# Optimization experiments

Measured on AMD Instinct MI355X. Metric: run time of the kernel, lower is better.

The kernel has to match this reference:

```python
import jax, jax.numpy as jnp
import numpy as np

B, L, D = 32, 256, 1024
ALIGN = 1024
FF = 2048
NUM_CLASSES = 3


def setup_inputs() -> dict:
    key = jax.random.key(0)
    ks = jax.random.split(key, 10)
    u = lambda k, shape: jax.random.uniform(k, shape, jnp.float32, -1.0, 1.0)
    return {
        "premises": jax.random.normal(ks[0], (B, L, D), jnp.float32),
        "hypotheses": jax.random.normal(ks[1], (B, L, D), jnp.float32),
        "W_F": u(ks[2], (D, ALIGN)),
        "W_G": u(ks[3], (2 * D, FF)),
        "W1": u(ks[4], (2 * FF, FF)) * 0.02,
        "b1": jnp.zeros((FF,), jnp.float32),
        "W2": u(ks[5], (FF, FF)) * 0.02,
        "b2": jnp.zeros((FF,), jnp.float32),
        "W3": u(ks[6], (FF, NUM_CLASSES)) * 0.02,
        "b3": jnp.zeros((NUM_CLASSES,), jnp.float32),
    }


def reference(premises, hypotheses, W_F, W_G, W1, b1, W2, b2, W3, b3):
    # ---- align: tanh-projected cross attention ----
    F_p = jnp.tanh(jnp.einsum("bpd,da->bpa", premises, W_F))      # [B,Lp,A]
    F_h = jnp.tanh(jnp.einsum("bhd,da->bha", hypotheses, W_F))    # [B,Lh,A]
    eijs = jnp.einsum("bpa,bha->bph", F_p, F_h)                   # [B,Lp,Lh]
    attn = jax.nn.softmax(eijs, axis=-1)                          # tf.nn.softmax: last axis
    betas = jnp.einsum("bph,bhd->bpd", attn, hypotheses)          # [B,Lp,D]
    alphas = jnp.einsum("bph,bpd->bhd", attn, premises)           # [B,Lh,D]

    # ---- compare (dropout is identity: p_keep = 1.0 at eval) ----
    V1 = jnp.tanh(jnp.concatenate([premises, betas], axis=2) @ W_G)    # [B,Lp,FF]
    V2 = jnp.tanh(jnp.concatenate([hypotheses, alphas], axis=2) @ W_G) # [B,Lh,FF]

    # ---- aggregate: sum-pool over sequence, concat ----
    agg = jnp.concatenate([V1.sum(axis=1), V2.sum(axis=1)], axis=1)    # [B,2*FF]

    # ---- classifier MLP ----
    a1 = jnp.tanh(agg @ W1 + b1)
    a2 = jnp.tanh(a1 @ W2 + b2)
    logits = a2 @ W3 + b3                                              # [B,3]
    return logits
```

## Files before the change

### kernel.cpp

```cpp
#include <hip/hip_runtime.h>
#include <hip/hip_bf16.h>
#include <stdint.h>


typedef __attribute__((ext_vector_type(8))) short    short8_t;
typedef __attribute__((ext_vector_type(4))) float    float4_t;
typedef __attribute__((ext_vector_type(8))) _Float16 half8_t;
typedef __attribute__((ext_vector_type(4))) _Float16 half4_t;

#define DEVI static __device__ __forceinline__

DEVI short f2bf(float f) {
  union { float f; unsigned u; } v; v.f = f;
  unsigned r = v.u + 0x7fffu + ((v.u >> 16) & 1u);
  return (short)(r >> 16);
}
DEVI float bf2f(short s) {
  union { unsigned u; float f; } v;
  v.u = ((unsigned)(unsigned short)s) << 16;
  return v.f;
}
DEVI void split2(float x, short& hi, short& lo) {
  hi = f2bf(x);
  lo = f2bf(x - bf2f(hi));
}
DEVI float fast_tanh(float x) {
  float e = __expf(2.0f * x);
  return 1.0f - 2.0f / (e + 1.0f);
}
DEVI void gload16(const void* g, void* l) {
  __builtin_amdgcn_global_load_lds(
      (const __attribute__((address_space(1))) void*)g,
      (__attribute__((address_space(3))) void*)l, 16, 0, 0);
}

template <int DO_TANH, int OUT_MODE>
__global__ __launch_bounds__(256) void gemm_nt_split(
    const short* __restrict__ Ah, const short* __restrict__ Al, int lda, long sA,
    const short* __restrict__ Bh, const short* __restrict__ Bl, int ldb, long sB,
    void* __restrict__ Ch, void* __restrict__ Cl, int ldc, long sC,
    int M, int K, int kslices)
{
  __shared__ __align__(16) short Ash[128][40];
  __shared__ __align__(16) short Asl[128][40];
  __shared__ __align__(16) short Bsh[128][40];
  __shared__ __align__(16) short Bsl[128][40];

  const int z  = blockIdx.z;
  const int zb = z / kslices;
  const int zk = z - zb * kslices;
  const int Ksub = K / kslices;
  const int kbeg = zk * Ksub, kend = kbeg + Ksub;

  Ah += (size_t)zb * sA;  Al += (size_t)zb * sA;
  Bh += (size_t)zb * sB;  Bl += (size_t)zb * sB;

  const int row0 = blockIdx.x * 128;
  const int col0 = blockIdx.y * 128;

  const int t    = threadIdx.x;
  const int lane = t & 63;
  const int wave = t >> 6;
  const int wr = wave >> 1, wc = wave & 1;
  const int m15 = lane & 15, q = lane >> 4;

  float4_t acc[4][4];
#pragma unroll
  for (int i = 0; i < 4; ++i)
#pragma unroll
    for (int j = 0; j < 4; ++j) acc[i][j] = (float4_t)0.0f;

  for (int k0 = kbeg; k0 < kend; k0 += 32) {
#pragma unroll
    for (int i = 0; i < 2; ++i) {
      int c  = t + 256 * i;
      int r  = c >> 2;
      int kc = (c & 3) << 3;
      size_t ao = (size_t)(row0 + r) * lda + k0 + kc;
      size_t bo = (size_t)(col0 + r) * ldb + k0 + kc;
      *(int4*)(&Ash[r][kc]) = *(const int4*)(Ah + ao);
      *(int4*)(&Asl[r][kc]) = *(const int4*)(Al + ao);
      *(int4*)(&Bsh[r][kc]) = *(const int4*)(Bh + bo);
      *(int4*)(&Bsl[r][kc]) = *(const int4*)(Bl + bo);
    }
    __syncthreads();

    short8_t ah[4], al[4];
#pragma unroll
    for (int i = 0; i < 4; ++i) {
      ah[i] = *(const short8_t*)(&Ash[wr * 64 + i * 16 + m15][q * 8]);
      al[i] = *(const short8_t*)(&Asl[wr * 64 + i * 16 + m15][q * 8]);
    }
#pragma unroll
    for (int j = 0; j < 4; ++j) {
      short8_t bh = *(const short8_t*)(&Bsh[wc * 64 + j * 16 + m15][q * 8]);
      short8_t bl = *(const short8_t*)(&Bsl[wc * 64 + j * 16 + m15][q * 8]);
#pragma unroll
      for (int i = 0; i < 4; ++i) {
        acc[i][j] = __builtin_amdgcn_mfma_f32_16x16x32_bf16(ah[i], bh, acc[i][j], 0, 0, 0);
        acc[i][j] = __builtin_amdgcn_mfma_f32_16x16x32_bf16(ah[i], bl, acc[i][j], 0, 0, 0);
        acc[i][j] = __builtin_amdgcn_mfma_f32_16x16x32_bf16(al[i], bh, acc[i][j], 0, 0, 0);
      }
    }
    __syncthreads();
  }

  short* Chs = (short*)Ch + (size_t)zb * sC;
  short* Cls = (short*)Cl + (size_t)zb * sC;
  float* Cf  = (float*)Ch + (size_t)zb * sC;
#pragma unroll
  for (int i = 0; i < 4; ++i) {
#pragma unroll
    for (int r = 0; r < 4; ++r) {
      int gm = row0 + wr * 64 + i * 16 + q * 4 + r;
      if (gm < M) {
#pragma unroll
        for (int j = 0; j < 4; ++j) {
          int gn = col0 + wc * 64 + j * 16 + m15;
          float v = acc[i][j][r];
          if (DO_TANH) v = fast_tanh(v);
          if (OUT_MODE == 0) {
            atomicAdd(&Cf[(size_t)gm * ldc + gn], v);
          } else {
            short hi, lo; split2(v, hi, lo);
            Chs[(size_t)gm * ldc + gn] = hi;
            Cls[(size_t)gm * ldc + gn] = lo;
          }
        }
      }
    }
  }
}

template <int MODE>
__global__ __launch_bounds__(256) void gemm_f16(
    const _Float16* __restrict__ A, int lda, long sA,
    const _Float16* __restrict__ B, int ldb, long sB,
    _Float16* __restrict__ C, int ldc, long sC,
    int K, float* __restrict__ agg)
{
  __shared__ __align__(16) _Float16 As[2 * 128 * 32];
  __shared__ __align__(16) _Float16 Bs[2 * 128 * 32];

  const int z = blockIdx.z;
  A += (size_t)z * sA;
  B += (size_t)z * sB;

  const int row0 = blockIdx.x * 128;
  const int col0 = blockIdx.y * 128;
  const int t = threadIdx.x, lane = t & 63, wave = t >> 6;
  const int wr = wave >> 1, wc = wave & 1;
  const int m15 = lane & 15, q = lane >> 4;

  const int srow = wave * 32 + (lane >> 2);
  const int cg   = ((lane & 3) ^ ((lane >> 3) & 3)) * 8;
  const _Float16* gA0 = A + (size_t)(row0 + srow) * lda + cg;
  const _Float16* gA1 = gA0 + (size_t)16 * lda;
  const _Float16* gB0 = B + (size_t)(col0 + srow) * ldb + cg;
  const _Float16* gB1 = gB0 + (size_t)16 * ldb;
  const _Float16* gA0b = gA0 + 32;
  const _Float16* gA1b = gA1 + 32;
  const _Float16* gB0b = gB0 + 32;
  const _Float16* gB1b = gB1 + 32;
  _Float16* lA0  = &As[(wave * 32) * 32];
  _Float16* lA1  = &As[(wave * 32 + 16) * 32];
  _Float16* lB0  = &Bs[(wave * 32) * 32];
  _Float16* lB1  = &Bs[(wave * 32 + 16) * 32];
  _Float16* lA0b = lA0 + 4096;
  _Float16* lA1b = lA1 + 4096;
  _Float16* lB0b = lB0 + 4096;
  _Float16* lB1b = lB1 + 4096;

  const int fs = (q ^ ((m15 >> 1) & 3)) * 8;
  int aoff[4], boff[4];
#pragma unroll
  for (int i = 0; i < 4; ++i) {
    aoff[i] = (wr * 64 + i * 16 + m15) * 32 + fs;
    boff[i] = (wc * 64 + i * 16 + m15) * 32 + fs;
  }

  float4_t acc[4][4];
#pragma unroll
  for (int i = 0; i < 4; ++i)
#pragma unroll
    for (int j = 0; j < 4; ++j) acc[i][j] = (float4_t)0.0f;

  for (int k0 = 0; k0 < K; k0 += 64) {
    gload16(gA0, lA0);  gload16(gA1, lA1);
    gload16(gB0, lB0);  gload16(gB1, lB1);
    gload16(gA0b, lA0b); gload16(gA1b, lA1b);
    gload16(gB0b, lB0b); gload16(gB1b, lB1b);
    gA0 += 64; gA1 += 64; gB0 += 64; gB1 += 64;
    gA0b += 64; gA1b += 64; gB0b += 64; gB1b += 64;
    __syncthreads();

#pragma unroll
    for (int h = 0; h < 2; ++h) {
      half8_t af[4], bfr[4];
#pragma unroll
      for (int i = 0; i < 4; ++i) af[i]  = *(const half8_t*)&As[h * 4096 + aoff[i]];
#pragma unroll
      for (int j = 0; j < 4; ++j) bfr[j] = *(const half8_t*)&Bs[h * 4096 + boff[j]];
#pragma unroll
      for (int i = 0; i < 4; ++i)
#pragma unroll
        for (int j = 0; j < 4; ++j)
          acc[i][j] = __builtin_amdgcn_mfma_f32_16x16x32_f16(af[i], bfr[j], acc[i][j], 0, 0, 0);
    }
    __syncthreads();
  }

  if (MODE == 2) {
    const int half_ = row0 >= 8192;
    const int b     = (row0 & 8191) >> 8;
#pragma unroll
    for (int j = 0; j < 4; ++j) {
      float s = 0.0f;
#pragma unroll
      for (int i = 0; i < 4; ++i)
#pragma unroll
        for (int r = 0; r < 4; ++r) s += fast_tanh(acc[i][j][r]);
      s += __shfl_xor(s, 16);
      s += __shfl_xor(s, 32);
      if (q == 0) {
        int col = col0 + wc * 64 + j * 16 + m15;
        atomicAdd(&agg[(size_t)b * 4096 + half_ * 2048 + col], s);
      }
    }
  } else {
    _Float16* Cp = C + (size_t)z * sC;
#pragma unroll
    for (int i = 0; i < 4; ++i)
#pragma unroll
      for (int r = 0; r < 4; ++r) {
        int gm = row0 + wr * 64 + i * 16 + q * 4 + r;
#pragma unroll
        for (int j = 0; j < 4; ++j) {
          int gn = col0 + wc * 64 + j * 16 + m15;
          Cp[(size_t)gm * ldc + gn] = (_Float16)acc[i][j][r];
        }
      }
  }
}

__global__ __launch_bounds__(256) void transpose_split(
    const float* __restrict__ in, short* __restrict__ oh, short* __restrict__ ol,
    int R, int C)
{
  __shared__ float tile[32][33];
  const int tx = threadIdx.x & 31, ty = threadIdx.x >> 5;
  const int c0 = blockIdx.x * 32, r0 = blockIdx.y * 32;
#pragma unroll
  for (int i = 0; i < 4; ++i) {
    int r = ty + i * 8;
    tile[r][tx] = in[(size_t)(r0 + r) * C + c0 + tx];
  }
  __syncthreads();
#pragma unroll
  for (int i = 0; i < 4; ++i) {
    int cc = ty + i * 8;
    float v = tile[tx][cc];
    short hi, lo; split2(v, hi, lo);
    size_t o = (size_t)(c0 + cc) * R + r0 + tx;
    oh[o] = hi;
    ol[o] = lo;
  }
}

__global__ __launch_bounds__(256) void transpose_f16(
    const float* __restrict__ in, _Float16* __restrict__ out, int R, int C)
{
  __shared__ float tile[32][33];
  const int tx = threadIdx.x & 31, ty = threadIdx.x >> 5;
  const int c0 = blockIdx.x * 32, r0 = blockIdx.y * 32;
#pragma unroll
  for (int i = 0; i < 4; ++i) {
    int r = ty + i * 8;
    tile[r][tx] = in[(size_t)(r0 + r) * C + c0 + tx];
  }
  __syncthreads();
#pragma unroll
  for (int i = 0; i < 4; ++i) {
    int cc = ty + i * 8;
    out[(size_t)(c0 + cc) * R + r0 + tx] = (_Float16)tile[tx][cc];
  }
}

__global__ __launch_bounds__(256) void transpose_f16_ph(
    const float* __restrict__ P, const float* __restrict__ Hh,
    _Float16* __restrict__ out)
{
  __shared__ float tile[32][33];
  const int zz = blockIdx.z;
  const float* in = (zz < 32 ? P : Hh) + (size_t)(zz & 31) * (256 * 1024);
  _Float16* o = out + (size_t)zz * (1024 * 256);
  const int tx = threadIdx.x & 31, ty = threadIdx.x >> 5;
  const int c0 = blockIdx.x * 32, r0 = blockIdx.y * 32;
#pragma unroll
  for (int i = 0; i < 4; ++i) {
    int r = ty + i * 8;
    tile[r][tx] = in[(size_t)(r0 + r) * 1024 + c0 + tx];
  }
  __syncthreads();
#pragma unroll
  for (int i = 0; i < 4; ++i) {
    int cc = ty + i * 8;
    o[(size_t)(c0 + cc) * 256 + r0 + tx] = (_Float16)tile[tx][cc];
  }
}

__global__ __launch_bounds__(256) void transpose_b2b(
    const short* __restrict__ in, short* __restrict__ out,
    int R, int C, long sIn, long sOut)
{
  __shared__ short tile[32][33];
  in  += (size_t)blockIdx.z * sIn;
  out += (size_t)blockIdx.z * sOut;
  const int tx = threadIdx.x & 31, ty = threadIdx.x >> 5;
  const int c0 = blockIdx.x * 32, r0 = blockIdx.y * 32;
#pragma unroll
  for (int i = 0; i < 4; ++i) {
    int r = ty + i * 8;
    tile[r][tx] = in[(size_t)(r0 + r) * C + c0 + tx];
  }
  __syncthreads();
#pragma unroll
  for (int i = 0; i < 4; ++i) {
    int cc = ty + i * 8;
    out[(size_t)(c0 + cc) * R + r0 + tx] = tile[tx][cc];
  }
}

__global__ __launch_bounds__(256) void conv_in(
    const float* __restrict__ P, const float* __restrict__ Hh,
    short* __restrict__ oh, short* __restrict__ ol, _Float16* __restrict__ cat)
{
  const int zz = blockIdx.z;
  const float* in = zz ? Hh : P;
  oh  += (size_t)zz * 8192 * 1024;
  ol  += (size_t)zz * 8192 * 1024;
  cat += (size_t)zz * 8192 * 2048;
  size_t i = ((size_t)blockIdx.x * 256 + threadIdx.x) * 4;
  float4 v = *(const float4*)&in[i];
  short4 h, l;
  split2(v.x, h.x, l.x); split2(v.y, h.y, l.y);
  split2(v.z, h.z, l.z); split2(v.w, h.w, l.w);
  *(short4*)&oh[i] = h;
  *(short4*)&ol[i] = l;
  size_t row = i >> 10;
  int col    = (int)(i & 1023);
  half4_t c16;
  c16.x = (_Float16)v.x; c16.y = (_Float16)v.y;
  c16.z = (_Float16)v.z; c16.w = (_Float16)v.w;
  *(half4_t*)&cat[row * 2048 + col] = c16;
}

__global__ __launch_bounds__(256) void conv_split(
    const float* __restrict__ in, short* __restrict__ oh, short* __restrict__ ol,
    int n)
{
  int i = (blockIdx.x * 256 + threadIdx.x) * 4;
  if (i < n) {
    float4 v = *(const float4*)&in[i];
    short4 h, l;
    split2(v.x, h.x, l.x); split2(v.y, h.y, l.y);
    split2(v.z, h.z, l.z); split2(v.w, h.w, l.w);
    *(short4*)&oh[i] = h;
    *(short4*)&ol[i] = l;
  }
}

__global__ __launch_bounds__(256) void zero_f32(float* __restrict__ p, int n)
{
  int i = blockIdx.x * 256 + threadIdx.x;
  if (i < n) p[i] = 0.0f;
}

__global__ __launch_bounds__(256) void softmax_rows(
    const float* __restrict__ e, _Float16* __restrict__ attn)
{
  const int row  = blockIdx.x * 4 + (threadIdx.x >> 6);
  const int lane = threadIdx.x & 63;
  const float4 v = *(const float4*)&e[(size_t)row * 256 + lane * 4];
  float m = fmaxf(fmaxf(v.x, v.y), fmaxf(v.z, v.w));
#pragma unroll
  for (int off = 32; off; off >>= 1) m = fmaxf(m, __shfl_xor(m, off));
  float e0 = __expf(v.x - m), e1 = __expf(v.y - m);
  float e2 = __expf(v.z - m), e3 = __expf(v.w - m);
  float s = e0 + e1 + e2 + e3;
#pragma unroll
  for (int off = 32; off; off >>= 1) s += __shfl_xor(s, off);
  float inv = 1.0f / s;
  half4_t o;
  o.x = (_Float16)(e0 * inv); o.y = (_Float16)(e1 * inv);
  o.z = (_Float16)(e2 * inv); o.w = (_Float16)(e3 * inv);
  *(half4_t*)&attn[(size_t)row * 256 + lane * 4] = o;
}

__global__ __launch_bounds__(256) void bias_tanh_split(
    const float* __restrict__ c, const float* __restrict__ bias,
    short* __restrict__ oh, short* __restrict__ ol, int n)
{
  int i = blockIdx.x * 256 + threadIdx.x;
  if (i < n) {
    float v = fast_tanh(c[i] + bias[i & 2047]);
    short hi, lo; split2(v, hi, lo);
    oh[i] = hi;
    ol[i] = lo;
  }
}

__global__ __launch_bounds__(256) void logits2(
    const float* __restrict__ c2f, const float* __restrict__ b2,
    const float* __restrict__ W3, const float* __restrict__ b3,
    float* __restrict__ out)
{
  const int b = blockIdx.x, t = threadIdx.x;
  float p0 = 0.f, p1 = 0.f, p2 = 0.f;
  for (int k = t; k < 2048; k += 256) {
    float a = fast_tanh(c2f[b * 2048 + k] + b2[k]);
    p0 += a * W3[k * 3 + 0];
    p1 += a * W3[k * 3 + 1];
    p2 += a * W3[k * 3 + 2];
  }
#pragma unroll
  for (int off = 32; off; off >>= 1) {
    p0 += __shfl_xor(p0, off);
    p1 += __shfl_xor(p1, off);
    p2 += __shfl_xor(p2, off);
  }
  __shared__ float red[4][3];
  if ((t & 63) == 0) {
    red[t >> 6][0] = p0; red[t >> 6][1] = p1; red[t >> 6][2] = p2;
  }
  __syncthreads();
  if (t < 3) out[b * 3 + t] = b3[t] + red[0][t] + red[1][t] + red[2][t] + red[3][t];
}

extern "C" void kernel_launch(void* const* d_in, const int* in_sizes, int n_in,
                              void* d_out, int out_size, void* d_ws, size_t ws_size,
                              hipStream_t stream) {
  (void)in_sizes; (void)n_in; (void)out_size; (void)ws_size;
  const float* P   = (const float*)d_in[0];
  const float* H   = (const float*)d_in[1];
  const float* W_F = (const float*)d_in[2];
  const float* W_G = (const float*)d_in[3];
  const float* W1  = (const float*)d_in[4];
  const float* b1  = (const float*)d_in[5];
  const float* W2  = (const float*)d_in[6];
  const float* b2  = (const float*)d_in[7];
  const float* W3  = (const float*)d_in[8];
  const float* b3  = (const float*)d_in[9];
  float* out = (float*)d_out;

  char* wsp = (char*)d_ws;
  auto alloc = [&](size_t bytes) {
    char* p = wsp;
    wsp += (bytes + 255) & ~(size_t)255;
    return p;
  };
  short*    Pp_h  = (short*)alloc(16384ull * 1024 * 2);
  short*    Pp_l  = (short*)alloc(16384ull * 1024 * 2);
  _Float16* Cat16 = (_Float16*)alloc(16384ull * 2048 * 2);
  short*    Fbuf  = (short*)alloc(32ull * 1024 * 1024 * 2);
  short*    WFT_h = (short*)alloc(1024ull * 1024 * 2);
  short*    WFT_l = (short*)alloc(1024ull * 1024 * 2);
  _Float16* WGT16 = (_Float16*)alloc(2048ull * 2048 * 2);
  float*    eijs  = (float*)alloc(32ull * 256 * 256 * 4);
  _Float16* attn  = (_Float16*)alloc(32ull * 256 * 256 * 2);
  _Float16* attnT = (_Float16*)alloc(32ull * 256 * 256 * 2);
  float*    agg   = (float*)alloc(32ull * 4096 * 4);
  short*    aggb_h= (short*)alloc(128ull * 4096 * 2);
  short*    aggb_l= (short*)alloc(128ull * 4096 * 2);
  float*    c1f   = (float*)alloc(32ull * 2048 * 4);
  float*    c2f   = (float*)alloc(32ull * 2048 * 4);
  short*    a1_h  = (short*)alloc(128ull * 2048 * 2);
  short*    a1_l  = (short*)alloc(128ull * 2048 * 2);

  short* F_h = Fbuf;
  short* F_l = Fbuf + 16384ull * 1024;
  _Float16* PHbT = (_Float16*)Fbuf;
  _Float16* PbT  = PHbT;
  _Float16* HbT  = PHbT + 32ull * 1024 * 256;
  short* W1T_h = Fbuf;
  short* W1T_l = Fbuf +  8ull * 1024 * 1024;
  short* W2T_h = Fbuf + 16ull * 1024 * 1024;
  short* W2T_l = Fbuf + 20ull * 1024 * 1024;

  conv_in<<<dim3(8192, 1, 2), 256, 0, stream>>>(P, H, Pp_h, Pp_l, Cat16);
  transpose_split<<<dim3(32, 32, 1), 256, 0, stream>>>(W_F, WFT_h, WFT_l, 1024, 1024);
  transpose_f16<<<dim3(64, 64, 1), 256, 0, stream>>>(W_G, WGT16, 2048, 2048);

  gemm_nt_split<1, 1><<<dim3(128, 8, 1), 256, 0, stream>>>(
      Pp_h, Pp_l, 1024, 0, WFT_h, WFT_l, 1024, 0,
      F_h, F_l, 1024, 0, 16384, 1024, 1);

  zero_f32<<<8192, 256, 0, stream>>>(eijs, 32 * 256 * 256);
  gemm_nt_split<0, 0><<<dim3(2, 2, 128), 256, 0, stream>>>(
      F_h, F_l, 1024, 256 * 1024,
      F_h + 8192ull * 1024, F_l + 8192ull * 1024, 1024, 256 * 1024,
      eijs, nullptr, 256, 65536, 256, 1024, 4);

  softmax_rows<<<2048, 256, 0, stream>>>(eijs, attn);
  transpose_b2b<<<dim3(8, 8, 32), 256, 0, stream>>>(
      (const short*)attn, (short*)attnT, 256, 256, 65536, 65536);
  transpose_f16_ph<<<dim3(32, 8, 64), 256, 0, stream>>>(P, H, PHbT);

  gemm_f16<1><<<dim3(2, 8, 32), 256, 0, stream>>>(
      attn, 256, 65536, HbT, 256, 1024 * 256,
      Cat16 + 1024, 2048, 256 * 2048, 256, nullptr);
  gemm_f16<1><<<dim3(2, 8, 32), 256, 0, stream>>>(
      attnT, 256, 65536, PbT, 256, 1024 * 256,
      Cat16 + 8192ull * 2048 + 1024, 2048, 256 * 2048, 256, nullptr);

  zero_f32<<<512, 256, 0, stream>>>(agg, 32 * 4096);
  gemm_f16<2><<<dim3(128, 16, 1), 256, 0, stream>>>(
      Cat16, 2048, 0, WGT16, 2048, 0, nullptr, 0, 0, 2048, agg);

  transpose_split<<<dim3(64, 128, 1), 256, 0, stream>>>(W1, W1T_h, W1T_l, 4096, 2048);
  transpose_split<<<dim3(64, 64, 1),  256, 0, stream>>>(W2, W2T_h, W2T_l, 2048, 2048);
  conv_split<<<128, 256, 0, stream>>>(agg, aggb_h, aggb_l, 32 * 4096);
  zero_f32<<<256, 256, 0, stream>>>(c1f, 32 * 2048);
  gemm_nt_split<0, 0><<<dim3(1, 16, 8), 256, 0, stream>>>(
      aggb_h, aggb_l, 4096, 0, W1T_h, W1T_l, 4096, 0,
      c1f, nullptr, 2048, 0, 32, 4096, 8);
  bias_tanh_split<<<256, 256, 0, stream>>>(c1f, b1, a1_h, a1_l, 32 * 2048);
  zero_f32<<<256, 256, 0, stream>>>(c2f, 32 * 2048);
  gemm_nt_split<0, 0><<<dim3(1, 16, 4), 256, 0, stream>>>(
      a1_h, a1_l, 2048, 0, W2T_h, W2T_l, 2048, 0,
      c2f, nullptr, 2048, 0, 32, 2048, 4);
  logits2<<<32, 256, 0, stream>>>(c2f, b2, W3, b3, out);
}
```

Measured before the change: 643.5 us.

## Swizzle split GEMM loads via global_load_lds, fuse input prep, replace MLP with fp32 skinny GEMM

The split-bf16 GEMM now stages tiles with direct global-to-LDS loads into an XOR-swizzled unpadded layout, removing the register round-trip and avoiding bank conflicts. The input conversion and the P/H transposes are merged into one kernel that reads the inputs once, and the two zeroing launches are combined. The classifier MLP drops the weight transposes, bf16 splitting and MFMA GEMMs in favour of a plain fp32 k-sliced skinny GEMM followed by reduction kernels that apply bias and tanh. This trades fewer launches and less traffic for a scalar FMA path with uncoalesced broadcast reads of A and a larger partial-sum buffer.

```diff
diff --git a/kernel.cpp b/kernel.cpp
--- a/kernel.cpp
+++ b/kernel.cpp
@@ -41,60 +41,74 @@
     void* __restrict__ Ch, void* __restrict__ Cl, int ldc, long sC,
     int M, int K, int kslices)
 {
-  __shared__ __align__(16) short Ash[128][40];
-  __shared__ __align__(16) short Asl[128][40];
-  __shared__ __align__(16) short Bsh[128][40];
-  __shared__ __align__(16) short Bsl[128][40];
+  __shared__ __align__(16) short Ash[128 * 32];
+  __shared__ __align__(16) short Asl[128 * 32];
+  __shared__ __align__(16) short Bsh[128 * 32];
+  __shared__ __align__(16) short Bsl[128 * 32];
 
   const int z  = blockIdx.z;
   const int zb = z / kslices;
   const int zk = z - zb * kslices;
   const int Ksub = K / kslices;
-  const int kbeg = zk * Ksub, kend = kbeg + Ksub;
+  const int kbeg = zk * Ksub;
 
   Ah += (size_t)zb * sA;  Al += (size_t)zb * sA;
   Bh += (size_t)zb * sB;  Bl += (size_t)zb * sB;
 
   const int row0 = blockIdx.x * 128;
   const int col0 = blockIdx.y * 128;
-
-  const int t    = threadIdx.x;
-  const int lane = t & 63;
-  const int wave = t >> 6;
+  const int t = threadIdx.x, lane = t & 63, wave = t >> 6;
   const int wr = wave >> 1, wc = wave & 1;
   const int m15 = lane & 15, q = lane >> 4;
 
+  const int srow = wave * 32 + (lane >> 2);
+  const int cg   = ((lane & 3) ^ ((lane >> 3) & 3)) * 8;
+  const short* gAh0 = Ah + (size_t)(row0 + srow) * lda + kbeg + cg;
+  const short* gAh1 = gAh0 + (size_t)16 * lda;
+  const short* gAl0 = Al + (size_t)(row0 + srow) * lda + kbeg + cg;
+  const short* gAl1 = gAl0 + (size_t)16 * lda;
+  const short* gBh0 = Bh + (size_t)(col0 + srow) * ldb + kbeg + cg;
+  const short* gBh1 = gBh0 + (size_t)16 * ldb;
+  const short* gBl0 = Bl + (size_t)(col0 + srow) * ldb + kbeg + cg;
+  const short* gBl1 = gBl0 + (size_t)16 * ldb;
+  short* lAh0 = &Ash[(wave * 32) * 32]; short* lAh1 = lAh0 + 16 * 32;
+  short* lAl0 = &Asl[(wave * 32) * 32]; short* lAl1 = lAl0 + 16 * 32;
+  short* lBh0 = &Bsh[(wave * 32) * 32]; short* lBh1 = lBh0 + 16 * 32;
+  short* lBl0 = &Bsl[(wave * 32) * 32]; short* lBl1 = lBl0 + 16 * 32;
+
+  const int fs = (q ^ ((m15 >> 1) & 3)) * 8;
+  int aoff[4], boff[4];
+#pragma unroll
+  for (int i = 0; i < 4; ++i) {
+    aoff[i] = (wr * 64 + i * 16 + m15) * 32 + fs;
+    boff[i] = (wc * 64 + i * 16 + m15) * 32 + fs;
+  }
+
   float4_t acc[4][4];
 #pragma unroll
   for (int i = 0; i < 4; ++i)
 #pragma unroll
     for (int j = 0; j < 4; ++j) acc[i][j] = (float4_t)0.0f;
 
-  for (int k0 = kbeg; k0 < kend; k0 += 32) {
-#pragma unroll
-    for (int i = 0; i < 2; ++i) {
-      int c  = t + 256 * i;
-      int r  = c >> 2;
-      int kc = (c & 3) << 3;
-      size_t ao = (size_t)(row0 + r) * lda + k0 + kc;
-      size_t bo = (size_t)(col0 + r) * ldb + k0 + kc;
-      *(int4*)(&Ash[r][kc]) = *(const int4*)(Ah + ao);
-      *(int4*)(&Asl[r][kc]) = *(const int4*)(Al + ao);
-      *(int4*)(&Bsh[r][kc]) = *(const int4*)(Bh + bo);
-      *(int4*)(&Bsl[r][kc]) = *(const int4*)(Bl + bo);
+  for (int it = 0; it < Ksub; it += 32) {
+    gload16(gAh0, lAh0); gload16(gAh1, lAh1);
+    gload16(gAl0, lAl0); gload16(gAl1, lAl1);
+    gload16(gBh0, lBh0); gload16(gBh1, lBh1);
+    gload16(gBl0, lBl0); gload16(gBl1, lBl1);
+    gAh0 += 32; gAh1 += 32; gAl0 += 32; gAl1 += 32;
+    gBh0 += 32; gBh1 += 32; gBl0 += 32; gBl1 += 32;
+    __syncthreads();
+
+    short8_t ah[4], al[4];
+#pragma unroll
+    for (int i = 0; i < 4; ++i) {
+      ah[i] = *(const short8_t*)&Ash[aoff[i]];
+      al[i] = *(const short8_t*)&Asl[aoff[i]];
     }
-    __syncthreads();
-
-    short8_t ah[4], al[4];
-#pragma unroll
-    for (int i = 0; i < 4; ++i) {
-      ah[i] = *(const short8_t*)(&Ash[wr * 64 + i * 16 + m15][q * 8]);
-      al[i] = *(const short8_t*)(&Asl[wr * 64 + i * 16 + m15][q * 8]);
-    }
 #pragma unroll
     for (int j = 0; j < 4; ++j) {
-      short8_t bh = *(const short8_t*)(&Bsh[wc * 64 + j * 16 + m15][q * 8]);
-      short8_t bl = *(const short8_t*)(&Bsl[wc * 64 + j * 16 + m15][q * 8]);
+      short8_t bh = *(const short8_t*)&Bsh[boff[j]];
+      short8_t bl = *(const short8_t*)&Bsl[boff[j]];
 #pragma unroll
       for (int i = 0; i < 4; ++i) {
         acc[i][j] = __builtin_amdgcn_mfma_f32_16x16x32_bf16(ah[i], bh, acc[i][j], 0, 0, 0);
@@ -243,6 +257,36 @@
   }
 }
 
+__global__ __launch_bounds__(256) void fused_in(
+    const float* __restrict__ P, const float* __restrict__ Hh,
+    short* __restrict__ oh, short* __restrict__ ol,
+    _Float16* __restrict__ cat, _Float16* __restrict__ phT)
+{
+  __shared__ float tile[32][33];
+  const int z = blockIdx.z;
+  const float* in = (z < 32 ? P : Hh) + (size_t)(z & 31) * (256 * 1024);
+  const int tx = threadIdx.x & 31, ty = threadIdx.x >> 5;
+  const int c0 = blockIdx.x * 32, r0 = blockIdx.y * 32;
+#pragma unroll
+  for (int i = 0; i < 4; ++i) {
+    int r = ty + i * 8;
+    float v = in[(size_t)(r0 + r) * 1024 + c0 + tx];
+    tile[r][tx] = v;
+    size_t grow = (size_t)z * 256 + r0 + r;
+    short hi, lo; split2(v, hi, lo);
+    oh[grow * 1024 + c0 + tx] = hi;
+    ol[grow * 1024 + c0 + tx] = lo;
+    cat[grow * 2048 + c0 + tx] = (_Float16)v;
+  }
+  __syncthreads();
+  _Float16* o = phT + (size_t)z * (1024 * 256);
+#pragma unroll
+  for (int i = 0; i < 4; ++i) {
+    int cc = ty + i * 8;
+    o[(size_t)(c0 + cc) * 256 + r0 + tx] = (_Float16)tile[tx][cc];
+  }
+}
+
 __global__ __launch_bounds__(256) void transpose_split(
     const float* __restrict__ in, short* __restrict__ oh, short* __restrict__ ol,
     int R, int C)
@@ -286,29 +330,6 @@
   }
 }
 
-__global__ __launch_bounds__(256) void transpose_f16_ph(
-    const float* __restrict__ P, const float* __restrict__ Hh,
-    _Float16* __restrict__ out)
-{
-  __shared__ float tile[32][33];
-  const int zz = blockIdx.z;
-  const float* in = (zz < 32 ? P : Hh) + (size_t)(zz & 31) * (256 * 1024);
-  _Float16* o = out + (size_t)zz * (1024 * 256);
-  const int tx = threadIdx.x & 31, ty = threadIdx.x >> 5;
-  const int c0 = blockIdx.x * 32, r0 = blockIdx.y * 32;
-#pragma unroll
-  for (int i = 0; i < 4; ++i) {
-    int r = ty + i * 8;
-    tile[r][tx] = in[(size_t)(r0 + r) * 1024 + c0 + tx];
-  }
-  __syncthreads();
-#pragma unroll
-  for (int i = 0; i < 4; ++i) {
-    int cc = ty + i * 8;
-    o[(size_t)(c0 + cc) * 256 + r0 + tx] = (_Float16)tile[tx][cc];
-  }
-}
-
 __global__ __launch_bounds__(256) void transpose_b2b(
     const short* __restrict__ in, short* __restrict__ out,
     int R, int C, long sIn, long sOut)
@@ -328,45 +349,6 @@
   for (int i = 0; i < 4; ++i) {
     int cc = ty + i * 8;
     out[(size_t)(c0 + cc) * R + r0 + tx] = tile[tx][cc];
-  }
-}
-
-__global__ __launch_bounds__(256) void conv_in(
-    const float* __restrict__ P, const float* __restrict__ Hh,
-    short* __restrict__ oh, short* __restrict__ ol, _Float16* __restrict__ cat)
-{
-  const int zz = blockIdx.z;
-  const float* in = zz ? Hh : P;
-  oh  += (size_t)zz * 8192 * 1024;
-  ol  += (size_t)zz * 8192 * 1024;
-  cat += (size_t)zz * 8192 * 2048;
-  size_t i = ((size_t)blockIdx.x * 256 + threadIdx.x) * 4;
-  float4 v = *(const float4*)&in[i];
-  short4 h, l;
-  split2(v.x, h.x, l.x); split2(v.y, h.y, l.y);
-  split2(v.z, h.z, l.z); split2(v.w, h.w, l.w);
-  *(short4*)&oh[i] = h;
-  *(short4*)&ol[i] = l;
-  size_t row = i >> 10;
-  int col    = (int)(i & 1023);
-  half4_t c16;
-  c16.x = (_Float16)v.x; c16.y = (_Float16)v.y;
-  c16.z = (_Float16)v.z; c16.w = (_Float16)v.w;
-  *(half4_t*)&cat[row * 2048 + col] = c16;
-}
-
-__global__ __launch_bounds__(256) void conv_split(
-    const float* __restrict__ in, short* __restrict__ oh, short* __restrict__ ol,
-    int n)
-{
-  int i = (blockIdx.x * 256 + threadIdx.x) * 4;
-  if (i < n) {
-    float4 v = *(const float4*)&in[i];
-    short4 h, l;
-    split2(v.x, h.x, l.x); split2(v.y, h.y, l.y);
-    split2(v.z, h.z, l.z); split2(v.w, h.w, l.w);
-    *(short4*)&oh[i] = h;
-    *(short4*)&ol[i] = l;
   }
 }
 
@@ -397,28 +379,50 @@
   *(half4_t*)&attn[(size_t)row * 256 + lane * 4] = o;
 }
 
-__global__ __launch_bounds__(256) void bias_tanh_split(
-    const float* __restrict__ c, const float* __restrict__ bias,
-    short* __restrict__ oh, short* __restrict__ ol, int n)
+__global__ __launch_bounds__(256) void skinny_gemm(
+    const float* __restrict__ A, int lda,
+    const float* __restrict__ W, int N, int Kslice,
+    float* __restrict__ part)
+{
+  const int n  = blockIdx.x * 256 + threadIdx.x;
+  const int k0 = blockIdx.y * Kslice;
+  float acc[32];
+#pragma unroll
+  for (int m = 0; m < 32; ++m) acc[m] = 0.0f;
+  for (int k = k0; k < k0 + Kslice; ++k) {
+    float w = W[(size_t)k * N + n];
+#pragma unroll
+    for (int m = 0; m < 32; ++m)
+      acc[m] = fmaf(A[m * lda + k], w, acc[m]);
+  }
+  float* pp = part + (size_t)blockIdx.y * 32 * N;
+#pragma unroll
+  for (int m = 0; m < 32; ++m) pp[(size_t)m * N + n] = acc[m];
+}
+
+__global__ __launch_bounds__(256) void reduce_bias_tanh(
+    const float* __restrict__ part, const float* __restrict__ bias,
+    float* __restrict__ outp, int n, int slices)
 {
   int i = blockIdx.x * 256 + threadIdx.x;
-  if (i < n) {
-    float v = fast_tanh(c[i] + bias[i & 2047]);
-    short hi, lo; split2(v, hi, lo);
-    oh[i] = hi;
-    ol[i] = lo;
-  }
-}
-
-__global__ __launch_bounds__(256) void logits2(
-    const float* __restrict__ c2f, const float* __restrict__ b2,
+  if (i >= n) return;
+  float s = bias[i & 2047];
+  for (int sl = 0; sl < slices; ++sl) s += part[(size_t)sl * n + i];
+  outp[i] = fast_tanh(s);
+}
+
+__global__ __launch_bounds__(256) void logits_red(
+    const float* __restrict__ part, const float* __restrict__ b2,
     const float* __restrict__ W3, const float* __restrict__ b3,
-    float* __restrict__ out)
+    float* __restrict__ out, int slices)
 {
   const int b = blockIdx.x, t = threadIdx.x;
   float p0 = 0.f, p1 = 0.f, p2 = 0.f;
   for (int k = t; k < 2048; k += 256) {
-    float a = fast_tanh(c2f[b * 2048 + k] + b2[k]);
+    float a = b2[k];
+    for (int sl = 0; sl < slices; ++sl)
+      a += part[((size_t)sl * 32 + b) * 2048 + k];
+    a = fast_tanh(a);
     p0 += a * W3[k * 3 + 0];
     p1 += a * W3[k * 3 + 1];
     p2 += a * W3[k * 3 + 2];
@@ -462,32 +466,26 @@
   short*    Pp_h  = (short*)alloc(16384ull * 1024 * 2);
   short*    Pp_l  = (short*)alloc(16384ull * 1024 * 2);
   _Float16* Cat16 = (_Float16*)alloc(16384ull * 2048 * 2);
+  _Float16* PHbT  = (_Float16*)alloc(64ull * 1024 * 256 * 2);
   short*    Fbuf  = (short*)alloc(32ull * 1024 * 1024 * 2);
   short*    WFT_h = (short*)alloc(1024ull * 1024 * 2);
   short*    WFT_l = (short*)alloc(1024ull * 1024 * 2);
   _Float16* WGT16 = (_Float16*)alloc(2048ull * 2048 * 2);
   float*    eijs  = (float*)alloc(32ull * 256 * 256 * 4);
+  float*    agg   = (float*)alloc(32ull * 4096 * 4);
   _Float16* attn  = (_Float16*)alloc(32ull * 256 * 256 * 2);
   _Float16* attnT = (_Float16*)alloc(32ull * 256 * 256 * 2);
-  float*    agg   = (float*)alloc(32ull * 4096 * 4);
-  short*    aggb_h= (short*)alloc(128ull * 4096 * 2);
-  short*    aggb_l= (short*)alloc(128ull * 4096 * 2);
-  float*    c1f   = (float*)alloc(32ull * 2048 * 4);
-  float*    c2f   = (float*)alloc(32ull * 2048 * 4);
-  short*    a1_h  = (short*)alloc(128ull * 2048 * 2);
-  short*    a1_l  = (short*)alloc(128ull * 2048 * 2);
 
   short* F_h = Fbuf;
   short* F_l = Fbuf + 16384ull * 1024;
-  _Float16* PHbT = (_Float16*)Fbuf;
-  _Float16* PbT  = PHbT;
-  _Float16* HbT  = PHbT + 32ull * 1024 * 256;
-  short* W1T_h = Fbuf;
-  short* W1T_l = Fbuf +  8ull * 1024 * 1024;
-  short* W2T_h = Fbuf + 16ull * 1024 * 1024;
-  short* W2T_l = Fbuf + 20ull * 1024 * 1024;
-
-  conv_in<<<dim3(8192, 1, 2), 256, 0, stream>>>(P, H, Pp_h, Pp_l, Cat16);
+  _Float16* PbT = PHbT;
+  _Float16* HbT = PHbT + 32ull * 1024 * 256;
+  float* c1p = (float*)Pp_h;
+  float* c2p = c1p + 32ull * 32 * 2048;
+  float* a1f = c2p + 32ull * 32 * 2048;
+
+  zero_f32<<<8704, 256, 0, stream>>>(eijs, 32 * 256 * 256 + 32 * 4096);
+  fused_in<<<dim3(32, 8, 64), 256, 0, stream>>>(P, H, Pp_h, Pp_l, Cat16, PHbT);
   transpose_split<<<dim3(32, 32, 1), 256, 0, stream>>>(W_F, WFT_h, WFT_l, 1024, 1024);
   transpose_f16<<<dim3(64, 64, 1), 256, 0, stream>>>(W_G, WGT16, 2048, 2048);
 
@@ -495,7 +493,6 @@
       Pp_h, Pp_l, 1024, 0, WFT_h, WFT_l, 1024, 0,
       F_h, F_l, 1024, 0, 16384, 1024, 1);
 
-  zero_f32<<<8192, 256, 0, stream>>>(eijs, 32 * 256 * 256);
   gemm_nt_split<0, 0><<<dim3(2, 2, 128), 256, 0, stream>>>(
       F_h, F_l, 1024, 256 * 1024,
       F_h + 8192ull * 1024, F_l + 8192ull * 1024, 1024, 256 * 1024,
@@ -504,7 +501,6 @@
   softmax_rows<<<2048, 256, 0, stream>>>(eijs, attn);
   transpose_b2b<<<dim3(8, 8, 32), 256, 0, stream>>>(
       (const short*)attn, (short*)attnT, 256, 256, 65536, 65536);
-  transpose_f16_ph<<<dim3(32, 8, 64), 256, 0, stream>>>(P, H, PHbT);
 
   gemm_f16<1><<<dim3(2, 8, 32), 256, 0, stream>>>(
       attn, 256, 65536, HbT, 256, 1024 * 256,
@@ -513,21 +509,11 @@
       attnT, 256, 65536, PbT, 256, 1024 * 256,
       Cat16 + 8192ull * 2048 + 1024, 2048, 256 * 2048, 256, nullptr);
 
-  zero_f32<<<512, 256, 0, stream>>>(agg, 32 * 4096);
   gemm_f16<2><<<dim3(128, 16, 1), 256, 0, stream>>>(
       Cat16, 2048, 0, WGT16, 2048, 0, nullptr, 0, 0, 2048, agg);
 
-  transpose_split<<<dim3(64, 128, 1), 256, 0, stream>>>(W1, W1T_h, W1T_l, 4096, 2048);
-  transpose_split<<<dim3(64, 64, 1),  256, 0, stream>>>(W2, W2T_h, W2T_l, 2048, 2048);
-  conv_split<<<128, 256, 0, stream>>>(agg, aggb_h, aggb_l, 32 * 4096);
-  zero_f32<<<256, 256, 0, stream>>>(c1f, 32 * 2048);
-  gemm_nt_split<0, 0><<<dim3(1, 16, 8), 256, 0, stream>>>(
-      aggb_h, aggb_l, 4096, 0, W1T_h, W1T_l, 4096, 0,
-      c1f, nullptr, 2048, 0, 32, 4096, 8);
-  bias_tanh_split<<<256, 256, 0, stream>>>(c1f, b1, a1_h, a1_l, 32 * 2048);
-  zero_f32<<<256, 256, 0, stream>>>(c2f, 32 * 2048);
-  gemm_nt_split<0, 0><<<dim3(1, 16, 4), 256, 0, stream>>>(
-      a1_h, a1_l, 2048, 0, W2T_h, W2T_l, 2048, 0,
-      c2f, nullptr, 2048, 0, 32, 2048, 4);
-  logits2<<<32, 256, 0, stream>>>(c2f, b2, W3, b3, out);
-}
+  skinny_gemm<<<dim3(8, 32), 256, 0, stream>>>(agg, 4096, W1, 2048, 128, c1p);
+  reduce_bias_tanh<<<256, 256, 0, stream>>>(c1p, b1, a1f, 32 * 2048, 32);
+  skinny_gemm<<<dim3(8, 32), 256, 0, stream>>>(a1f, 2048, W2, 2048, 64, c2p);
+  logits_red<<<32, 256, 0, stream>>>(c2p, b2, W3, b3, out, 32);
+}
```

Measured after the change: 812.0 us. 1.26x slower.
